# Kernel tuning notes

Measured on AMD Instinct MI355X. Metric: run time of the kernel, lower is better.

## Reference

```python
import jax, jax.numpy as jnp
import numpy as np

B, C2, H, W = 4, 1024, 64, 64  # features have 2*input_dim channels
CH = C2 // 2                   # 512 = input_dim
HID = CH // 4                  # 128 = hidden_channels


def setup_inputs() -> dict:
    key = jax.random.key(0)
    ks = jax.random.split(key, 6)
    left = jax.random.normal(ks[0], (B, C2, H, W), dtype=jnp.float32)
    right = jax.random.normal(ks[1], (B, C2, H, W), dtype=jnp.float32)
    # 1x1 conv params (weight [out,in], bias [out]) for query/reference projections
    Wq = jax.random.normal(ks[2], (HID, CH), dtype=jnp.float32) * 0.02
    bq = jax.random.normal(ks[3], (HID,), dtype=jnp.float32) * 0.02
    Wk = jax.random.normal(ks[4], (HID, CH), dtype=jnp.float32) * 0.02
    bk = jax.random.normal(ks[5], (HID,), dtype=jnp.float32) * 0.02
    return {"left_features": left, "right_features": right, "Wq": Wq, "bq": bq, "Wk": Wk, "bk": bk}


def _co_attention(qf, rf, Wq, bq, Wk, bk):
    # 1x1 convs == per-pixel channel matmuls
    Q = jnp.einsum('bchw,oc->bohw', qf, Wq) + bq[None, :, None, None]   # [B,HID,H,W]
    K = jnp.einsum('bchw,oc->bohw', rf, Wk) + bk[None, :, None, None]   # [B,HID,H,W]
    b, c, h, w = Q.shape
    Kf = K.reshape(b, c, h * w)                                          # [B,HID,P]
    V = rf.reshape(rf.shape[0], rf.shape[1], h * w)                      # [B,CH,P]
    # attention_map: einsum('bcij,bckl->bijkl') then flatten (kl) == contract channels
    attn = jnp.einsum('bcij,bcp->bijp', Q, Kf)                           # [B,H,W,P]
    attn = jax.nn.softmax(attn, axis=3)
    return jnp.einsum('bijp,bcp->bcij', attn, V)                         # [B,CH,H,W]


def _homo(qf, rf):
    weights = jax.nn.softmax(qf - rf, axis=1)  # softmax over channels
    return rf * weights


def _get_both_differences(q, r, Wq, bq, Wk, bk):
    c = q.shape[1] // 2
    q_orig, q_trans = q[:, :c], q[:, c:]
    r_orig = r[:, :c]
    cross = _co_attention(q_orig, r_orig, Wq, bq, Wk, bk)
    reduce = _homo(q_orig, q_trans)
    return jnp.concatenate([q_orig, cross + reduce], axis=1)


def reference(left_features, right_features, Wq, bq, Wk, bk):
    left_out = _get_both_differences(left_features, right_features, Wq, bq, Wk, bk)
    right_out = _get_both_differences(right_features, left_features, Wq, bq, Wk, bk)
    return (left_out, right_out)
```

## Files before the change

### kernel.cpp

```cpp
#include <hip/hip_runtime.h>
#include <hip/hip_bf16.h>

#define NB 4
#define LOG2E 1.4426950408889634f

typedef unsigned short u16;
typedef __attribute__((ext_vector_type(8))) short bf16x8;
typedef __attribute__((ext_vector_type(4))) float f32x4;

static __device__ __forceinline__ float bf2f(u16 u) {
    union { float f; unsigned v; } x; x.v = ((unsigned)u) << 16; return x.f;
}
static __device__ __forceinline__ u16 f2bf(float f) {
    unsigned v = __builtin_bit_cast(unsigned, f);
    return (u16)((v + 0x7FFFu + ((v >> 16) & 1u)) >> 16);
}
static __device__ __forceinline__ void gload_lds16(const u16* g, u16* l) {
    __builtin_amdgcn_global_load_lds(
        (const __attribute__((address_space(1))) unsigned*)(const void*)g,
        (__attribute__((address_space(3))) unsigned*)(void*)l, 16, 0, 0);
}

__global__ void k_wcvt(const float* __restrict__ Wq, const float* __restrict__ Wk,
                       u16* __restrict__ Wbq, u16* __restrict__ Wbk) {
    int i = blockIdx.x * 1024 + threadIdx.x;
    Wbq[i] = f2bf(Wq[i]);
    Wbk[i] = f2bf(Wk[i]);
}

__global__ __launch_bounds__(256) void k_cvtf(
        const float* __restrict__ L, const float* __restrict__ R,
        u16* __restrict__ Lb, u16* __restrict__ Rb,
        u16* __restrict__ web, float* __restrict__ sumsH, float* __restrict__ out) {
    __shared__ float pred[4][1024];
    int idx = blockIdx.x;
    int sb = idx & 7, pseg = (idx >> 3) & 3, cpart = idx >> 5;
    int side = sb & 1, b = sb >> 1;
    int osb = side * 4 + b;
    const float* src = (side ? R : L) + (size_t)b * 1024 * 4096;
    u16* lbbase = (side ? Rb : Lb) + (size_t)b * 512 * 4096;
    int tid = threadIdx.x, wv = tid >> 6, lane = tid & 63;
    int p0 = pseg * 1024;
    int cA = cpart * 8 + wv * 2;
#pragma unroll
    for (int s = 0; s < 4; s++) {
        int p = p0 + s * 256 + lane * 4;
        float4 sm = {0.f, 0.f, 0.f, 0.f};
#pragma unroll
        for (int cc = 0; cc < 2; cc++) {
            int c = cA + cc;
            float4 a = *reinterpret_cast<const float4*>(src + (size_t)c * 4096 + p);
            float4 t = *reinterpret_cast<const float4*>(src + (size_t)(512 + c) * 4096 + p);
            ushort4 ub;
            ub.x = f2bf(a.x); ub.y = f2bf(a.y); ub.z = f2bf(a.z); ub.w = f2bf(a.w);
            *reinterpret_cast<ushort4*>(lbbase + (size_t)c * 4096 + p) = ub;
            *reinterpret_cast<float4*>(out + ((size_t)osb * 1024 + c) * 4096 + p) = a;
            float4 e;
            e.x = exp2f((a.x - t.x) * LOG2E);
            e.y = exp2f((a.y - t.y) * LOG2E);
            e.z = exp2f((a.z - t.z) * LOG2E);
            e.w = exp2f((a.w - t.w) * LOG2E);
            sm.x += e.x; sm.y += e.y; sm.z += e.z; sm.w += e.w;
            ushort4 wb_;
            wb_.x = f2bf(t.x * e.x); wb_.y = f2bf(t.y * e.y);
            wb_.z = f2bf(t.z * e.z); wb_.w = f2bf(t.w * e.w);
            *reinterpret_cast<ushort4*>(web + ((size_t)osb * 512 + c) * 4096 + p) = wb_;
        }
        *reinterpret_cast<float4*>(&pred[wv][s * 256 + lane * 4]) = sm;
    }
    __syncthreads();
    {
        float4 t0 = *reinterpret_cast<const float4*>(&pred[0][tid * 4]);
        float4 t1 = *reinterpret_cast<const float4*>(&pred[1][tid * 4]);
        float4 t2 = *reinterpret_cast<const float4*>(&pred[2][tid * 4]);
        float4 t3 = *reinterpret_cast<const float4*>(&pred[3][tid * 4]);
        float4 tot;
        tot.x = (t0.x + t1.x) + (t2.x + t3.x);
        tot.y = (t0.y + t1.y) + (t2.y + t3.y);
        tot.z = (t0.z + t1.z) + (t2.z + t3.z);
        tot.w = (t0.w + t1.w) + (t2.w + t3.w);
        *reinterpret_cast<float4*>(
            sumsH + ((size_t)cpart * 8 + osb) * 4096 + p0 + tid * 4) = tot;
    }
}

__global__ __launch_bounds__(256) void k_hsum(const float* __restrict__ sumsH,
                                              float* __restrict__ hinv) {
    int i = blockIdx.x * 256 + threadIdx.x;
    float4 tot = {0.f, 0.f, 0.f, 0.f};
    for (int cp = 0; cp < 64; cp++) {
        float4 v = *reinterpret_cast<const float4*>(sumsH + (size_t)cp * 8 * 4096 + (size_t)i * 4);
        tot.x += v.x; tot.y += v.y; tot.z += v.z; tot.w += v.w;
    }
    float4 r = {1.0f / tot.x, 1.0f / tot.y, 1.0f / tot.z, 1.0f / tot.w};
    *reinterpret_cast<float4*>(hinv + (size_t)i * 4) = r;
}

__global__ void k_cvt(const float* __restrict__ L, const float* __restrict__ R,
                      u16* __restrict__ Lb, u16* __restrict__ Rb, float* __restrict__ out) {
    int i = blockIdx.x * 256 + threadIdx.x;
    int pq = i & 1023;
    int c = (i >> 10) & 511;
    int b = (i >> 19) & 3;
    int side = i >> 21;
    const float* src = (side ? R : L) + ((long)(b * 1024 + c) << 12) + (pq << 2);
    float4 v = *reinterpret_cast<const float4*>(src);
    ushort4 u;
    u.x = f2bf(v.x); u.y = f2bf(v.y); u.z = f2bf(v.z); u.w = f2bf(v.w);
    *reinterpret_cast<ushort4*>((side ? Rb : Lb) + ((long)(b * 512 + c) << 12) + (pq << 2)) = u;
    *reinterpret_cast<float4*>(out + ((long)(side * 4 + b) * 1024 + c) * 4096 + (pq << 2)) = v;
}

__global__ __launch_bounds__(256) void k_proj(
        const u16* __restrict__ Lb, const u16* __restrict__ Rb,
        const u16* __restrict__ Wbq, const u16* __restrict__ Wbk,
        const float* __restrict__ bq, const float* __restrict__ bk,
        u16* __restrict__ QL, u16* __restrict__ KL,
        u16* __restrict__ QR, u16* __restrict__ KR) {
    __shared__ u16 XT[2][64 * 40];
    int pj = blockIdx.x & 15, pt = blockIdx.x >> 4;
    int ty = pj >> 2, b = pj & 3;
    const u16* src; const u16* Wb; const float* bias; u16* dst;
    if (ty == 0)      { src = Lb; Wb = Wbq; bias = bq; dst = QL; }
    else if (ty == 1) { src = Rb; Wb = Wbk; bias = bk; dst = KL; }
    else if (ty == 2) { src = Rb; Wb = Wbq; bias = bq; dst = QR; }
    else              { src = Lb; Wb = Wbk; bias = bk; dst = KR; }
    const u16* X = src + (long)b * 512 * 4096 + pt * 64;
    int tid = threadIdx.x;
    int wv = __builtin_amdgcn_readfirstlane(tid >> 6);
    int lane = tid & 63, g = lane >> 4, li = lane & 15;

    f32x4 acc[8];
#pragma unroll
    for (int ob = 0; ob < 8; ob++)
#pragma unroll
        for (int r = 0; r < 4; r++) acc[ob][r] = bias[ob * 16 + g * 4 + r];

    int c_r = tid >> 3, j = tid & 7;
    bf16x8 gx = *reinterpret_cast<const bf16x8*>(X + (long)c_r * 4096 + j * 8);
#pragma unroll
    for (int k = 0; k < 8; k++) XT[0][(j * 8 + k) * 40 + c_r] = (u16)gx[k];
    __syncthreads();

    for (int cc = 0; cc < 16; cc++) {
        int buf = cc & 1;
        bf16x8 gn;
        if (cc < 15)
            gn = *reinterpret_cast<const bf16x8*>(X + (long)(cc * 32 + 32 + c_r) * 4096 + j * 8);
        bf16x8 xb = *reinterpret_cast<const bf16x8*>(&XT[buf][(wv * 16 + li) * 40 + g * 8]);
#pragma unroll
        for (int ob = 0; ob < 8; ob++) {
            bf16x8 aw = *reinterpret_cast<const bf16x8*>(Wb + (long)(ob * 16 + li) * 512 + cc * 32 + g * 8);
            acc[ob] = __builtin_amdgcn_mfma_f32_16x16x32_bf16(aw, xb, acc[ob], 0, 0, 0);
        }
        if (cc < 15) {
#pragma unroll
            for (int k = 0; k < 8; k++) XT[buf ^ 1][(j * 8 + k) * 40 + c_r] = (u16)gn[k];
        }
        __syncthreads();
    }
    u16* d = dst + ((long)b * 4096 + pt * 64 + wv * 16 + li) * 128;
#pragma unroll
    for (int ob = 0; ob < 8; ob++) {
        uint2 w;
        w.x = (unsigned)f2bf(acc[ob][0]) | ((unsigned)f2bf(acc[ob][1]) << 16);
        w.y = (unsigned)f2bf(acc[ob][2]) | ((unsigned)f2bf(acc[ob][3]) << 16);
        *reinterpret_cast<uint2*>(d + ob * 16 + g * 4) = w;
    }
}

__global__ __launch_bounds__(512, 2) void k_qk(
        const u16* __restrict__ QL, const u16* __restrict__ KL,
        const u16* __restrict__ QR, const u16* __restrict__ KR,
        u16* __restrict__ P, float* __restrict__ sums,
        int bd0, int bdMask, int bdShift) {
    __shared__ u16 Kl[3][8192];
    __shared__ u16 Ps[4096];
    __shared__ float sred[4][2][16];
    int bdl = (int)blockIdx.x & bdMask;
    int rest = (int)blockIdx.x >> bdShift;
    int qtile = rest & 63;
    int ph0 = rest >> 6;
    int bd = bd0 + bdl, dir = bd & 1, b = bd >> 1;
    const u16* Qt = (dir ? QR : QL) + (size_t)b * 4096 * 128;
    const u16* Kt = (dir ? KR : KL) + (size_t)b * 4096 * 128;
    u16* Pbd = P + ((size_t)bdl << 24);
    int q0 = qtile * 64;
    int tid = threadIdx.x;
    int wv = __builtin_amdgcn_readfirstlane(tid >> 6);
    int lane = tid & 63, g = lane >> 4, li = lane & 15;
    int qt = wv >> 1, phw = wv & 1;

#define STAGE_K(BUF, PT)                                                                   \
    {                                                                                      \
        _Pragma("unroll") for (int r0 = 0; r0 < 2; r0++) {                                 \
            int o = r0 * 8192 + tid * 16;                                                  \
            int row = o >> 8, w = o & 255;                                                 \
            int sw = (w ^ ((row & 7) << 4)) >> 1;                                          \
            gload_lds16(Kt + (((size_t)((PT) * 64 + row)) << 7) + sw,                      \
                        &Kl[BUF][r0 * 4096 + wv * 512]);                                   \
        }                                                                                  \
    }

    bf16x8 qf[4];
#pragma unroll
    for (int hc = 0; hc < 4; hc++)
        qf[hc] = *reinterpret_cast<const bf16x8*>(
            Qt + (size_t)(q0 + qt * 16 + li) * 128 + hc * 32 + g * 8);
    float psum = 0.f;
    STAGE_K(0, ph0 * 32)
    STAGE_K(1, ph0 * 32 + 1)

    int cur = 0;
    for (int tt = 0; tt < 32; tt++) {
        int pt = ph0 * 32 + tt;
        if (tt == 0)       asm volatile("s_waitcnt vmcnt(2) lgkmcnt(0)\n\ts_barrier" ::: "memory");
        else if (tt == 1)  asm volatile("s_waitcnt vmcnt(3) lgkmcnt(0)\n\ts_barrier" ::: "memory");
        else if (tt == 31) asm volatile("s_waitcnt vmcnt(2) lgkmcnt(0)\n\ts_barrier" ::: "memory");
        else               asm volatile("s_waitcnt vmcnt(4) lgkmcnt(0)\n\ts_barrier" ::: "memory");
        if (tt < 30) {
            int stg = cur + 2; if (stg >= 3) stg -= 3;
            STAGE_K(stg, pt + 2)
        }
        f32x4 sv[2];
        sv[0] = (f32x4){0.f, 0.f, 0.f, 0.f};
        sv[1] = (f32x4){0.f, 0.f, 0.f, 0.f};
        __builtin_amdgcn_s_setprio(1);
#pragma unroll
        for (int ps = 0; ps < 2; ps++) {
            int row = phw * 32 + ps * 16 + li;
            unsigned rb = (unsigned)row * 256;
            unsigned sz = (unsigned)((row & 7) << 4);
#pragma unroll
            for (int hc = 0; hc < 4; hc++) {
                bf16x8 kf = *reinterpret_cast<const bf16x8*>(
                    (char*)Kl[cur] + rb + (((unsigned)(hc * 64 + g * 16)) ^ sz));
                sv[ps] = __builtin_amdgcn_mfma_f32_16x16x32_bf16(kf, qf[hc], sv[ps], 0, 0, 0);
            }
        }
        __builtin_amdgcn_s_setprio(0);
        int qrow = qt * 16 + li;
        unsigned qsz = (unsigned)((qrow & 7) << 4);
#pragma unroll
        for (int ps = 0; ps < 2; ps++) {
            float e0 = exp2f(sv[ps][0] * LOG2E);
            float e1 = exp2f(sv[ps][1] * LOG2E);
            float e2 = exp2f(sv[ps][2] * LOG2E);
            float e3 = exp2f(sv[ps][3] * LOG2E);
            psum += (e0 + e1) + (e2 + e3);
            uint2 pk;
            pk.x = (unsigned)f2bf(e0) | ((unsigned)f2bf(e1) << 16);
            pk.y = (unsigned)f2bf(e2) | ((unsigned)f2bf(e3) << 16);
            unsigned off = (unsigned)qrow * 128 +
                           (((unsigned)(phw * 64 + ps * 32 + g * 8)) ^ qsz);
            *reinterpret_cast<uint2*>((char*)Ps + off) = pk;
        }
        asm volatile("s_waitcnt lgkmcnt(0)\n\ts_barrier" ::: "memory");
        {
            uint4 d = *reinterpret_cast<const uint4*>((char*)Ps + tid * 16);
            *reinterpret_cast<uint4*>(
                Pbd + ((size_t)(qtile * 64 + pt) << 12) + tid * 8) = d;
        }
        cur = (cur + 1 == 3) ? 0 : cur + 1;
    }
    psum += __shfl_xor(psum, 16);
    psum += __shfl_xor(psum, 32);
    if (lane < 16) sred[qt][phw][li] = psum;
    __syncthreads();
    if (phw == 0 && lane < 16) {
        float s = sred[qt][0][li] + sred[qt][1][li];
        sums[((size_t)ph0 * 8 + bd) * 4096 + q0 + qt * 16 + li] = s;
    }
#undef STAGE_K
}

template<int FUSEH>
__global__ __launch_bounds__(256, 1) void k_pv(
        const u16* __restrict__ Lb, const u16* __restrict__ Rb,
        const u16* __restrict__ P, const float* __restrict__ sums,
        const u16* __restrict__ web, const float* __restrict__ hinvArr,
        float* __restrict__ out, int bd0, int bdMask, int bdShift) {
    __shared__ u16 Tl[3][2][8192];
    int bdl = (int)blockIdx.x & bdMask;
    int idx = (int)blockIdx.x >> bdShift;
    int mtile = idx & 3;
    int ntile = idx >> 2;
    int bd = bd0 + bdl, dir = bd & 1, b = bd >> 1;
    int osb = dir * 4 + b;
    const u16* V = (dir ? Lb : Rb) + (size_t)b * 512 * 4096;
    const u16* Pbd = P + ((size_t)bdl << 24);
    int q0 = ntile * 128, c0 = mtile * 128, qt0 = ntile * 2;
    int tid = threadIdx.x;
    int wv = __builtin_amdgcn_readfirstlane(tid >> 6);
    int lane = tid & 63, g = lane >> 4, li = lane & 15;
    int wr = wv >> 1, wc = wv & 1;

#define STAGE_PV(BUF, T)                                                                   \
    {                                                                                      \
        _Pragma("unroll") for (int r0 = 0; r0 < 4; r0++) {                                 \
            int o = r0 * 4096 + tid * 16;                                                  \
            int row = o >> 7, w = o & 127;                                                 \
            int sw = (w ^ ((row & 7) << 4)) >> 1;                                          \
            gload_lds16(V + (((size_t)(c0 + row)) << 12) + (T) * 64 + sw,                  \
                        &Tl[BUF][0][r0 * 2048 + wv * 512]);                                \
            gload_lds16(Pbd + (((size_t)((qt0 + (r0 >> 1)) * 64 + (T))) << 12) +           \
                            (r0 & 1) * 2048 + tid * 8,                                     \
                        &Tl[BUF][1][r0 * 2048 + wv * 512]);                                \
        }                                                                                  \
    }

    f32x4 acc[4][4];
#pragma unroll
    for (int i = 0; i < 4; i++)
#pragma unroll
        for (int j = 0; j < 4; j++) acc[i][j] = (f32x4){0.f, 0.f, 0.f, 0.f};

    STAGE_PV(0, 0)
    STAGE_PV(1, 1)

    int cur = 0;
    for (int t = 0; t < 64; t++) {
        if (t < 63) asm volatile("s_waitcnt vmcnt(8) lgkmcnt(0)\n\ts_barrier" ::: "memory");
        else        asm volatile("s_waitcnt vmcnt(0) lgkmcnt(0)\n\ts_barrier" ::: "memory");
        if (t < 62) {
            int stg = cur + 2; if (stg >= 3) stg -= 3;
            STAGE_PV(stg, t + 2)
        }
        bf16x8 af[4][2], bf[4][2];
#pragma unroll
        for (int mi = 0; mi < 4; mi++) {
            int row = wr * 64 + mi * 16 + li;
            unsigned rb = (unsigned)row * 128, sz = (unsigned)((row & 7) << 4);
#pragma unroll
            for (int kk = 0; kk < 2; kk++)
                af[mi][kk] = *reinterpret_cast<const bf16x8*>(
                    (char*)Tl[cur][0] + rb + (((unsigned)(kk * 64 + g * 16)) ^ sz));
        }
#pragma unroll
        for (int ni = 0; ni < 4; ni++) {
            int row = wc * 64 + ni * 16 + li;
            unsigned rb = (unsigned)row * 128, sz = (unsigned)((row & 7) << 4);
#pragma unroll
            for (int kk = 0; kk < 2; kk++)
                bf[ni][kk] = *reinterpret_cast<const bf16x8*>(
                    (char*)Tl[cur][1] + rb + (((unsigned)(kk * 64 + g * 16)) ^ sz));
        }
        __builtin_amdgcn_s_setprio(1);
#pragma unroll
        for (int kk = 0; kk < 2; kk++)
#pragma unroll
            for (int mi = 0; mi < 4; mi++)
#pragma unroll
                for (int ni = 0; ni < 4; ni++)
                    acc[mi][ni] = __builtin_amdgcn_mfma_f32_16x16x32_bf16(
                        af[mi][kk], bf[ni][kk], acc[mi][ni], 0, 0, 0);
        __builtin_amdgcn_s_setprio(0);
        cur = (cur + 1 == 3) ? 0 : cur + 1;
    }

    float* obase = out + ((size_t)osb * 1024 + 512) * 4096;
    const u16* wb = web + (size_t)osb * 512 * 4096;
#pragma unroll
    for (int ni = 0; ni < 4; ni++) {
        int q = q0 + wc * 64 + ni * 16 + li;
        float s0 = sums[(size_t)bd * 4096 + q];
        float s1 = sums[((size_t)8 + bd) * 4096 + q];
        float linv = 1.0f / (s0 + s1);
        float hinv = 0.f;
        if (FUSEH) hinv = hinvArr[(size_t)osb * 4096 + q];
#pragma unroll
        for (int mi = 0; mi < 4; mi++) {
            int c = c0 + wr * 64 + mi * 16 + g * 4;
#pragma unroll
            for (int r = 0; r < 4; r++) {
                float v = acc[mi][ni][r] * linv;
                if (FUSEH) v += bf2f(wb[(size_t)(c + r) * 4096 + q]) * hinv;
                obase[(size_t)(c + r) * 4096 + q] = v;
            }
        }
    }
#undef STAGE_PV
}

__global__ __launch_bounds__(256) void k_homo(const float* __restrict__ L,
                                              const float* __restrict__ R,
                                              float* __restrict__ out) {
    __shared__ float4 red[16][16];
    int sb = blockIdx.x & 7, pblk = blockIdx.x >> 3;
    int side = sb & 1, b = sb >> 1;
    const float* src = (side ? R : L) + (long)b * 1024 * 4096;
    float* o = out + (long)(side * 4 + b) * 1024 * 4096;
    int p4 = threadIdx.x & 15, cg = threadIdx.x >> 4;
    int p = pblk * 64 + p4 * 4;
    const float* qo = src + p;
    const float* qt = src + (long)512 * 4096 + p;
    float4 sm = {0.f, 0.f, 0.f, 0.f};
    for (int c = cg * 32; c < cg * 32 + 32; c++) {
        float4 a = *reinterpret_cast<const float4*>(qo + (long)c * 4096);
        float4 t = *reinterpret_cast<const float4*>(qt + (long)c * 4096);
        sm.x += exp2f((a.x - t.x) * LOG2E);
        sm.y += exp2f((a.y - t.y) * LOG2E);
        sm.z += exp2f((a.z - t.z) * LOG2E);
        sm.w += exp2f((a.w - t.w) * LOG2E);
    }
    red[cg][p4] = sm;
    __syncthreads();
    float4 tot = {0.f, 0.f, 0.f, 0.f};
#pragma unroll
    for (int gR = 0; gR < 16; gR++) {
        float4 v = red[gR][p4];
        tot.x += v.x; tot.y += v.y; tot.z += v.z; tot.w += v.w;
    }
    float4 rinv = {1.0f / tot.x, 1.0f / tot.y, 1.0f / tot.z, 1.0f / tot.w};
    for (int c = cg * 32; c < cg * 32 + 32; c++) {
        float4 a = *reinterpret_cast<const float4*>(qo + (long)c * 4096);
        float4 t = *reinterpret_cast<const float4*>(qt + (long)c * 4096);
        float4* op = reinterpret_cast<float4*>(o + (long)(512 + c) * 4096 + p);
        float4 cur = *op;
        cur.x += t.x * exp2f((a.x - t.x) * LOG2E) * rinv.x;
        cur.y += t.y * exp2f((a.y - t.y) * LOG2E) * rinv.y;
        cur.z += t.z * exp2f((a.z - t.z) * LOG2E) * rinv.z;
        cur.w += t.w * exp2f((a.w - t.w) * LOG2E) * rinv.w;
        *op = cur;
    }
}

extern "C" void kernel_launch(void* const* d_in, const int* in_sizes, int n_in,
                              void* d_out, int out_size, void* d_ws, size_t ws_size,
                              hipStream_t stream) {
    const float* L  = (const float*)d_in[0];
    const float* R  = (const float*)d_in[1];
    const float* Wq = (const float*)d_in[2];
    const float* bq = (const float*)d_in[3];
    const float* Wk = (const float*)d_in[4];
    const float* bk = (const float*)d_in[5];
    float* out = (float*)d_out;
    char* ws = (char*)d_ws;

    size_t off = 0;
    u16* Wbq = (u16*)(ws + off); off += (size_t)128 * 512 * 2;
    u16* Wbk = (u16*)(ws + off); off += (size_t)128 * 512 * 2;
    u16* QL = (u16*)(ws + off); off += (size_t)NB * 4096 * 128 * 2;
    u16* KL = (u16*)(ws + off); off += (size_t)NB * 4096 * 128 * 2;
    u16* QR = (u16*)(ws + off); off += (size_t)NB * 4096 * 128 * 2;
    u16* KR = (u16*)(ws + off); off += (size_t)NB * 4096 * 128 * 2;
    u16* Lb = (u16*)(ws + off); off += (size_t)NB * 512 * 4096 * 2;
    u16* Rb = (u16*)(ws + off); off += (size_t)NB * 512 * 4096 * 2;
    float* sums = (float*)(ws + off); off += (size_t)2 * 8 * 4096 * 4;
    float* hinv = (float*)(ws + off); off += (size_t)8 * 4096 * 4;
    size_t off_nofuse = off;
    float* sumsH = (float*)(ws + off); off += (size_t)64 * 8 * 4096 * 4;
    u16* web = (u16*)(ws + off); off += (size_t)8 * 512 * 4096 * 2;
    off = (off + 255) & ~(size_t)255;
    size_t pchunk4 = (size_t)4 * 4096 * 4096 * 2;

    k_wcvt <<<64, 1024, 0, stream>>>(Wq, Wk, Wbq, Wbk);

    if (ws_size >= off + pchunk4) {
        u16* Pb = (u16*)(ws + off);
        k_cvtf <<<2048, 256, 0, stream>>>(L, R, Lb, Rb, web, sumsH, out);
        k_hsum <<<32,   256, 0, stream>>>(sumsH, hinv);
        k_proj <<<1024, 256, 0, stream>>>(Lb, Rb, Wbq, Wbk, bq, bk, QL, KL, QR, KR);
        for (int c = 0; c < 2; c++) {
            k_qk    <<<512, 512, 0, stream>>>(QL, KL, QR, KR, Pb, sums, c * 4, 3, 2);
            k_pv<1> <<<512, 256, 0, stream>>>(Lb, Rb, Pb, sums, web, hinv, out, c * 4, 3, 2);
        }
    } else {
        int nbd, bdShift;
        size_t poff = (off_nofuse + 255) & ~(size_t)255;
        if (ws_size >= poff + pchunk4) { nbd = 4; bdShift = 2; }
        else                           { nbd = 1; bdShift = 0; }
        int bdMask = nbd - 1, nchunk = 8 / nbd;
        u16* Pb = (u16*)(ws + poff);
        k_cvt  <<<16384, 256, 0, stream>>>(L, R, Lb, Rb, out);
        k_proj <<<1024,  256, 0, stream>>>(Lb, Rb, Wbq, Wbk, bq, bk, QL, KL, QR, KR);
        for (int c = 0; c < nchunk; c++) {
            k_qk    <<<nbd * 128, 512, 0, stream>>>(QL, KL, QR, KR, Pb, sums,
                                                    c * nbd, bdMask, bdShift);
            k_pv<0> <<<nbd * 128, 256, 0, stream>>>(Lb, Rb, Pb, sums, web, hinv, out,
                                                    c * nbd, bdMask, bdShift);
        }
        k_homo <<<512, 256, 0, stream>>>(L, R, out);
    }
}
```

Baseline: 461.2 us.

## Remap blocks to XCDs and switch PV kernel to double-buffered two-block occupancy

When four batch-direction slots are processed, the block-index decode in both the QK and PV kernels changes so that blocks landing on the same XCD share the same batch/direction and K/P data, which should improve L2 locality. The PV kernel drops from a triple-buffered LDS pipeline with one block per CU to a double-buffered one (64KB LDS) with launch bounds allowing two blocks per CU. The wider latency hiding now has to come from the second resident block rather than a deeper prefetch, and each iteration now waits for all outstanding loads before its barrier.

```diff
diff --git a/kernel.cpp b/kernel.cpp
--- a/kernel.cpp
+++ b/kernel.cpp
@@ -177,10 +177,15 @@
     __shared__ u16 Kl[3][8192];
     __shared__ u16 Ps[4096];
     __shared__ float sred[4][2][16];
-    int bdl = (int)blockIdx.x & bdMask;
-    int rest = (int)blockIdx.x >> bdShift;
-    int qtile = rest & 63;
-    int ph0 = rest >> 6;
+    int bdl, qtile, ph0;
+    if (bdMask == 3) {
+        int xcd = (int)blockIdx.x & 7;
+        bdl = xcd >> 1; ph0 = xcd & 1; qtile = (int)blockIdx.x >> 3;
+    } else {
+        bdl = (int)blockIdx.x & bdMask;
+        int rest = (int)blockIdx.x >> bdShift;
+        qtile = rest & 63; ph0 = rest >> 6;
+    }
     int bd = bd0 + bdl, dir = bd & 1, b = bd >> 1;
     const u16* Qt = (dir ? QR : QL) + (size_t)b * 4096 * 128;
     const u16* Kt = (dir ? KR : KL) + (size_t)b * 4096 * 128;
@@ -275,14 +280,21 @@
 }
 
 template<int FUSEH>
-__global__ __launch_bounds__(256, 1) void k_pv(
+__global__ __launch_bounds__(256, 2) void k_pv(
         const u16* __restrict__ Lb, const u16* __restrict__ Rb,
         const u16* __restrict__ P, const float* __restrict__ sums,
         const u16* __restrict__ web, const float* __restrict__ hinvArr,
         float* __restrict__ out, int bd0, int bdMask, int bdShift) {
-    __shared__ u16 Tl[3][2][8192];
-    int bdl = (int)blockIdx.x & bdMask;
-    int idx = (int)blockIdx.x >> bdShift;
+    __shared__ u16 Tl[2][2][8192];
+    int bdl, idx;
+    if (bdMask == 3) {
+        int xcd = (int)blockIdx.x & 7;
+        bdl = xcd >> 1;
+        idx = (((int)blockIdx.x >> 3) << 1) | (xcd & 1);
+    } else {
+        bdl = (int)blockIdx.x & bdMask;
+        idx = (int)blockIdx.x >> bdShift;
+    }
     int mtile = idx & 3;
     int ntile = idx >> 2;
     int bd = bd0 + bdl, dir = bd & 1, b = bd >> 1;
@@ -316,16 +328,11 @@
         for (int j = 0; j < 4; j++) acc[i][j] = (f32x4){0.f, 0.f, 0.f, 0.f};
 
     STAGE_PV(0, 0)
-    STAGE_PV(1, 1)
-
-    int cur = 0;
+
     for (int t = 0; t < 64; t++) {
-        if (t < 63) asm volatile("s_waitcnt vmcnt(8) lgkmcnt(0)\n\ts_barrier" ::: "memory");
-        else        asm volatile("s_waitcnt vmcnt(0) lgkmcnt(0)\n\ts_barrier" ::: "memory");
-        if (t < 62) {
-            int stg = cur + 2; if (stg >= 3) stg -= 3;
-            STAGE_PV(stg, t + 2)
-        }
+        asm volatile("s_waitcnt vmcnt(0) lgkmcnt(0)\n\ts_barrier" ::: "memory");
+        if (t < 63) STAGE_PV((t + 1) & 1, t + 1)
+        int buf = t & 1;
         bf16x8 af[4][2], bf[4][2];
 #pragma unroll
         for (int mi = 0; mi < 4; mi++) {
@@ -334,7 +341,7 @@
 #pragma unroll
             for (int kk = 0; kk < 2; kk++)
                 af[mi][kk] = *reinterpret_cast<const bf16x8*>(
-                    (char*)Tl[cur][0] + rb + (((unsigned)(kk * 64 + g * 16)) ^ sz));
+                    (char*)Tl[buf][0] + rb + (((unsigned)(kk * 64 + g * 16)) ^ sz));
         }
 #pragma unroll
         for (int ni = 0; ni < 4; ni++) {
@@ -343,7 +350,7 @@
 #pragma unroll
             for (int kk = 0; kk < 2; kk++)
                 bf[ni][kk] = *reinterpret_cast<const bf16x8*>(
-                    (char*)Tl[cur][1] + rb + (((unsigned)(kk * 64 + g * 16)) ^ sz));
+                    (char*)Tl[buf][1] + rb + (((unsigned)(kk * 64 + g * 16)) ^ sz));
         }
         __builtin_amdgcn_s_setprio(1);
 #pragma unroll
@@ -355,7 +362,6 @@
                     acc[mi][ni] = __builtin_amdgcn_mfma_f32_16x16x32_bf16(
                         af[mi][kk], bf[ni][kk], acc[mi][ni], 0, 0, 0);
         __builtin_amdgcn_s_setprio(0);
-        cur = (cur + 1 == 3) ? 0 : cur + 1;
     }
 
     float* obase = out + ((size_t)osb * 1024 + 512) * 4096;
```

Result: faster. 406.6 us (-11.8%).
